# Performance work log

Hardware: AMD Instinct MI355X
Metric: run time of the kernel (lower is better)

The kernel has to match this reference:

```python
import jax, jax.numpy as jnp
import numpy as np

EPS = 1e-5

def inorm(x):
    # instance norm over time (last) axis; torch.std is unbiased (ddof=1)
    m = jnp.mean(x, axis=-1, keepdims=True)
    s = jnp.sqrt(jnp.var(x, axis=-1, ddof=1, keepdims=True))
    return (x - m) / (s + EPS)

def tinorm(x):
    # time-wise instance norm: normalize over channel axis (dim=1)
    m = jnp.mean(x, axis=1, keepdims=True)
    s = jnp.sqrt(jnp.var(x, axis=1, ddof=1, keepdims=True))
    return (x - m) / (s + EPS)

def adaptive_norm(src, trg, wq, wk, wv, norm_fn):
    # src, trg: [B,C,T]; wq/wk/wv: [out,in] as in nn.Linear
    temp = src.shape[1] ** 0.5
    q = jnp.einsum('bct,oc->bto', norm_fn(src), wq)        # [B,Ts,C]
    k = jnp.einsum('bct,oc->bto', norm_fn(trg), wk)        # [B,Tt,C]
    v = jnp.einsum('bct,oc->bto', trg, wv)                 # [B,Tt,C]
    attn = jax.nn.softmax(jnp.einsum('bsc,btc->bst', q / temp, k), axis=-1)
    mean = jnp.einsum('bst,btc->bsc', attn, v)             # attn-weighted mean
    var = jax.nn.relu(jnp.einsum('bst,btc->bsc', attn, v * v) - mean * mean)
    mean_c = jnp.mean(mean, axis=1)[:, :, None]            # [B,C,1]
    std_c = jnp.sqrt(jnp.mean(var, axis=1))[:, :, None]    # [B,C,1]
    return std_c * inorm(src) + mean_c

def sap(x, w, b):
    # self-attention pooling over axis 1; x: [B,N,C], w: [C], b: [1]
    a = jax.nn.softmax(jnp.einsum('bnc,c->bn', x, w) + b, axis=-1)
    return jnp.einsum('bnc,bn->bc', x, a)

def setup_inputs():
    key = jax.random.key(0)
    ks = jax.random.split(key, 24)
    B, C, Ts, Tt, S = 4, 512, 2048, 2048, 2048
    sc = 1.0 / np.sqrt(C).astype(np.float32)
    return {
        'src': jax.random.normal(ks[0], (B, C, Ts), jnp.float32),
        'trg': jax.random.normal(ks[1], (B, C, Tt), jnp.float32),
        'means': jax.random.normal(ks[2], (B, S, C), jnp.float32),
        'stds': jax.random.uniform(ks[3], (B, S, C), jnp.float32),
        'wq_t': jax.random.normal(ks[4], (C, C), jnp.float32) * sc,
        'wk_t': jax.random.normal(ks[5], (C, C), jnp.float32) * sc,
        'wv_t': jax.random.normal(ks[6], (C, C), jnp.float32) * sc,
        'wq_c': jax.random.normal(ks[7], (C, C), jnp.float32) * sc,
        'wk_c': jax.random.normal(ks[8], (C, C), jnp.float32) * sc,
        'wv_c': jax.random.normal(ks[9], (C, C), jnp.float32) * sc,
        'conv1_w': jax.random.normal(ks[10], (C, 2 * C), jnp.float32) * sc,
        'conv1_b': jax.random.normal(ks[11], (C,), jnp.float32) * 0.02,
        'conv2_w': jax.random.normal(ks[12], (C, C, 3), jnp.float32) * sc,
        'bn_g': jax.random.uniform(ks[13], (C,), jnp.float32, 0.5, 1.5),
        'bn_b': jax.random.normal(ks[14], (C,), jnp.float32) * 0.05,
        'bn_m': jax.random.normal(ks[15], (C,), jnp.float32) * 0.1,
        'bn_v': jax.random.uniform(ks[16], (C,), jnp.float32, 0.5, 1.5),
        'msap_w': jax.random.normal(ks[17], (C,), jnp.float32) * sc,
        'msap_b': jax.random.normal(ks[18], (1,), jnp.float32) * 0.02,
        'ssap_w': jax.random.normal(ks[19], (C,), jnp.float32) * sc,
        'ssap_b': jax.random.normal(ks[20], (1,), jnp.float32) * 0.02,
    }

def reference(src, trg, means, stds, wq_t, wk_t, wv_t, wq_c, wk_c, wv_c,
              conv1_w, conv1_b, conv2_w, bn_g, bn_b, bn_m, bn_v,
              msap_w, msap_b, ssap_w, ssap_b):
    src1 = adaptive_norm(src, trg, wq_t, wk_t, wv_t, tinorm)   # TAN
    src2 = adaptive_norm(src, trg, wq_c, wk_c, wv_c, inorm)    # CAN
    x = jnp.concatenate([src1, src2], axis=1)                  # [B,2C,T]
    # conv1: kernel_size=1 -> pointwise GEMM
    x = jnp.einsum('bct,oc->bot', x, conv1_w) + conv1_b[None, :, None]
    # conv2: Conv1d(k=3, pad=1, bias=False) + BatchNorm1d(eval) + ReLU
    x = jax.lax.conv_general_dilated(x, conv2_w, (1,), 'SAME',
                                     dimension_numbers=('NCH', 'OIH', 'NCH'))
    x = (x - bn_m[None, :, None]) * jax.lax.rsqrt(bn_v[None, :, None] + EPS)
    x = x * bn_g[None, :, None] + bn_b[None, :, None]
    x = jax.nn.relu(x)
    # GLAN
    mean = sap(means, msap_w, msap_b)[:, :, None]              # [B,C,1]
    std = sap(stds, ssap_w, ssap_b)[:, :, None]                # [B,C,1]
    return inorm(x) * std + mean
```

## Files before the change

kernel.cpp:

```cpp
#include <hip/hip_runtime.h>
#include <cstdint>
#include <cstddef>

#define B_ 4
#define C_ 512
#define T_ 2048
#define S_ 2048
#define EPSF 1e-5f

typedef __bf16 bf16;
typedef __attribute__((ext_vector_type(8))) __bf16 bf16x8;
typedef __attribute__((ext_vector_type(4))) float f32x4;

__device__ __forceinline__ bf16 f2b(float f){ return (bf16)f; }
__device__ __forceinline__ float b2f(bf16 h){ return (float)h; }

__device__ __forceinline__ void gl_lds16(const void* g, void* l){
  __builtin_amdgcn_global_load_lds((__attribute__((address_space(1))) void*)(g),
                                   (__attribute__((address_space(3))) void*)(l), 16, 0, 0);
}

__device__ __forceinline__ float wave_sum(float v){
#pragma unroll
  for (int o = 32; o; o >>= 1) v += __shfl_xor(v, o, 64);
  return v;
}
__device__ __forceinline__ float wave_max(float v){
#pragma unroll
  for (int o = 32; o; o >>= 1) v = fmaxf(v, __shfl_xor(v, o, 64));
  return v;
}

template<int EPI, int TNW>
__global__ void __launch_bounds__(256) gemm_nt(
    const bf16* __restrict__ A, const bf16* __restrict__ Bm, void* __restrict__ Cout,
    int K, int lda, int ldb, int ldc,
    long long sA, long long sB, long long sC, long long sCb,
    int zdivA, int zmodB, float scale,
    const float* __restrict__ rs, const float* __restrict__ rsh,
    const float* __restrict__ cbias,
    float* __restrict__ osum, float* __restrict__ osum2, long long sRs)
{
  constexpr int TN = TNW*32;
  __shared__ alignas(16) bf16 lA[128*64];
  __shared__ alignas(16) bf16 lB[TN*64];
  __shared__ float l_sh[128];
  const int tid = threadIdx.x;
  int z, m0, n0;
  if (EPI == 3) {
    const int id = blockIdx.x;
    z = id & 7;
    const int r = id >> 3;
    n0 = (r & 3) * TN;
    m0 = (r >> 2) * 128;
  } else {
    z = blockIdx.z; m0 = blockIdx.y*128; n0 = blockIdx.x*TN;
  }
  const bf16* Ab = A + (long long)(z / zdivA) * sA;
  const bf16* Bb = Bm + (long long)(z % zmodB) * sB;
  const int lane = tid & 63, wvi = tid >> 6;
  const int wm = wvi >> 1, wn = wvi & 1;

  f32x4 acc[4][TNW] = {};
  f32x4 accL[4] = {};
  bf16x8 vone;
#pragma unroll
  for (int j = 0; j < 8; ++j) vone[j] = f2b(1.f);

  const int lrow = tid >> 3;
  const int lcol = ((tid ^ lrow) & 7) * 8;
  const bf16* pa = Ab + (long long)(m0 + lrow)*lda + lcol;
  const bf16* pb = Bb + (long long)(n0 + lrow)*ldb + lcol;
  char* sa = (char*)lA + tid*16;
  char* sb = (char*)lB + tid*16;

  for (int k0 = 0; k0 < K; k0 += 64) {
#pragma unroll
    for (int it = 0; it < 4; ++it)
      gl_lds16(pa + (long long)it*32*lda + k0, sa + it*4096);
#pragma unroll
    for (int it = 0; it < TNW; ++it)
      gl_lds16(pb + (long long)it*32*ldb + k0, sb + it*4096);
    __syncthreads();
#pragma unroll
    for (int ks = 0; ks < 2; ++ks) {
      const int kq = ks*4 + (lane >> 4);
      bf16x8 af[4], bfr[TNW];
#pragma unroll
      for (int mt = 0; mt < 4; ++mt) {
        int r = wm*64 + mt*16 + (lane & 15);
        af[mt] = *(const bf16x8*)&lA[r*64 + ((kq ^ (r & 7))*8)];
      }
#pragma unroll
      for (int nt = 0; nt < TNW; ++nt) {
        int r = wn*(TNW*16) + nt*16 + (lane & 15);
        bfr[nt] = *(const bf16x8*)&lB[r*64 + ((kq ^ (r & 7))*8)];
      }
#pragma unroll
      for (int mt = 0; mt < 4; ++mt)
#pragma unroll
        for (int nt = 0; nt < TNW; ++nt)
          acc[mt][nt] = __builtin_amdgcn_mfma_f32_16x16x32_bf16(af[mt], bfr[nt], acc[mt][nt], 0, 0, 0);
      if (EPI == 3 && wn == 0) {
#pragma unroll
        for (int mt = 0; mt < 4; ++mt)
          accL[mt] = __builtin_amdgcn_mfma_f32_16x16x32_bf16(af[mt], vone, accL[mt], 0, 0, 0);
      }
    }
    __syncthreads();
  }

  if (EPI == 3) {
    if (wn == 0 && (lane & 15) == 0) {
#pragma unroll
      for (int mt = 0; mt < 4; ++mt)
#pragma unroll
        for (int i = 0; i < 4; ++i)
          l_sh[wm*64 + mt*16 + (lane >> 4)*4 + i] = accL[mt][i];
    }
    __syncthreads();
    if (n0 == 0 && tid < 128)
      ((float*)Cout)[(long long)z*sC + m0 + tid] = l_sh[tid];
    float linv[4][4];
#pragma unroll
    for (int mt = 0; mt < 4; ++mt)
#pragma unroll
      for (int i = 0; i < 4; ++i)
        linv[mt][i] = 1.f / l_sh[wm*64 + mt*16 + (lane >> 4)*4 + i];
    float* red1 = (float*)lA;
    float* red2 = red1 + 4*TNW*16;
    float s1[TNW], s2[TNW];
#pragma unroll
    for (int nt = 0; nt < TNW; ++nt) {
      s1[nt] = 0.f; s2[nt] = 0.f;
#pragma unroll
      for (int mt = 0; mt < 4; ++mt)
#pragma unroll
        for (int i = 0; i < 4; ++i) {
          float v = acc[mt][nt][i] * linv[mt][i];
          s1[nt] += v; s2[nt] += v*v;
        }
      s1[nt] += __shfl_xor(s1[nt], 16, 64);
      s1[nt] += __shfl_xor(s1[nt], 32, 64);
      s2[nt] += __shfl_xor(s2[nt], 16, 64);
      s2[nt] += __shfl_xor(s2[nt], 32, 64);
    }
    if (lane < 16) {
#pragma unroll
      for (int nt = 0; nt < TNW; ++nt) {
        red1[(wvi*TNW + nt)*16 + lane] = s1[nt];
        red2[(wvi*TNW + nt)*16 + lane] = s2[nt];
      }
    }
    __syncthreads();
    if (tid < 2*TN) {
      const int which = tid >= TN;
      const int col = tid - which*TN;
      const int wn2 = col / (TNW*16), rem = col % (TNW*16);
      const float* rr = which ? red2 : red1;
      float v = rr[wn2*(TNW*16) + rem] + rr[(2+wn2)*(TNW*16) + rem];
      float* dst = which ? osum2 : osum;
      atomicAdd(&dst[sCb*z + n0 + col], v);
    }
    return;
  }

  const int cr = (lane >> 4)*4, cc = lane & 15;
#pragma unroll
  for (int mt = 0; mt < 4; ++mt) {
#pragma unroll
    for (int i = 0; i < 4; ++i) {
      const int mm = m0 + wm*64 + mt*16 + cr + i;
      float rsum = 0.f, rsum2 = 0.f;
#pragma unroll
      for (int nt = 0; nt < TNW; ++nt) {
        const int nn = n0 + wn*(TNW*16) + nt*16 + cc;
        float v = acc[mt][nt][i];
        const long long co = sC*z + (long long)mm*ldc + nn;
        if (EPI == 0) {
          v *= scale;
          if (cbias) v += cbias[sCb*z + nn];
          ((bf16*)Cout)[co] = f2b(v);
        } else if (EPI == 2) {
          v = fmaxf(v*rs[mm] + rsh[mm], 0.f);
          ((float*)Cout)[co] = v;
          rsum += v; rsum2 += v*v;
        } else if (EPI == 5) {
          ((bf16*)Cout)[co] = f2b(__expf(v));
        }
      }
      if (EPI == 2) {
        rsum += __shfl_xor(rsum, 1, 64); rsum += __shfl_xor(rsum, 2, 64);
        rsum += __shfl_xor(rsum, 4, 64); rsum += __shfl_xor(rsum, 8, 64);
        rsum2 += __shfl_xor(rsum2, 1, 64); rsum2 += __shfl_xor(rsum2, 2, 64);
        rsum2 += __shfl_xor(rsum2, 4, 64); rsum2 += __shfl_xor(rsum2, 8, 64);
        if (cc == 0) {
          atomicAdd(&osum[(long long)z*sRs + mm], rsum);
          atomicAdd(&osum2[(long long)z*sRs + mm], rsum2);
        }
      }
    }
  }
}

__global__ void __launch_bounds__(256) row_stats_k(const float* __restrict__ X1,
    const float* __restrict__ X2, float* __restrict__ Mo, float* __restrict__ So, int n1)
{
  __shared__ float r1[4], r2[4];
  const int row = blockIdx.x;
  const float* x = (row < n1) ? X1 + (long long)row*T_ : X2 + (long long)(row-n1)*T_;
  float s1 = 0.f, s2 = 0.f;
  for (int i = threadIdx.x; i < T_; i += 256){ float v = x[i]; s1 += v; s2 += v*v; }
  s1 = wave_sum(s1); s2 = wave_sum(s2);
  const int lane = threadIdx.x & 63, w = threadIdx.x >> 6;
  if (!lane){ r1[w] = s1; r2[w] = s2; }
  __syncthreads();
  if (threadIdx.x == 0){
    s1 = r1[0]+r1[1]+r1[2]+r1[3];
    s2 = r2[0]+r2[1]+r2[2]+r2[3];
    float m = s1 * (1.f/T_);
    float var = (s2 - s1*m) * (1.f/(T_-1));
    Mo[row] = m; So[row] = sqrtf(fmaxf(var, 0.f));
  }
}

__global__ void __launch_bounds__(256) col_stats_k(const float* __restrict__ src,
    const float* __restrict__ trg, float* __restrict__ Mo, float* __restrict__ So)
{
  __shared__ float r1[4][64], r2[4][64];
  const int z = blockIdx.y, t0 = blockIdx.x*64;
  const float* X = (z < B_) ? src : trg;
  const int b = z & (B_-1);
  const int tl = threadIdx.x & 63, cg = threadIdx.x >> 6;
  float s1 = 0.f, s2 = 0.f;
  for (int c = cg; c < C_; c += 4) {
    float v = X[((long long)b*C_ + c)*T_ + t0 + tl];
    s1 += v; s2 += v*v;
  }
  r1[cg][tl] = s1; r2[cg][tl] = s2;
  __syncthreads();
  if (cg == 0) {
    s1 = r1[0][tl]+r1[1][tl]+r1[2][tl]+r1[3][tl];
    s2 = r2[0][tl]+r2[1][tl]+r2[2][tl]+r2[3][tl];
    float m = s1 * (1.f/C_);
    float var = (s2 - s1*m) * (1.f/(C_-1));
    Mo[z*T_ + t0 + tl] = m;
    So[z*T_ + t0 + tl] = sqrtf(fmaxf(var, 0.f));
  }
}

__global__ void __launch_bounds__(256) transform_k(const float* __restrict__ src,
    const float* __restrict__ trg,
    const float* __restrict__ tnm, const float* __restrict__ tns,
    const float* __restrict__ inm, const float* __restrict__ ins,
    bf16* __restrict__ NSt, bf16* __restrict__ NSc,
    bf16* __restrict__ NTt, bf16* __restrict__ NTc, bf16* __restrict__ TTr)
{
  __shared__ float tile[32][33];
  const int z = blockIdx.z, t0 = blockIdx.x*32, c0 = blockIdx.y*32;
  const int is_t = z >= B_, b = z & (B_-1);
  const float* X = is_t ? trg : src;
  const int tx = threadIdx.x, ty = threadIdx.y;
#pragma unroll
  for (int r = 0; r < 4; ++r) {
    int ci = ty + r*8;
    tile[ci][tx] = X[((long long)b*C_ + c0 + ci)*T_ + t0 + tx];
  }
  __syncthreads();
#pragma unroll
  for (int r = 0; r < 4; ++r) {
    int tj = ty + r*8, ci = tx;
    float v = tile[ci][tj];
    int gt = t0 + tj, gc = c0 + ci;
    float a = (v - tnm[z*T_ + gt]) / (tns[z*T_ + gt] + EPSF);
    float d = (v - inm[z*C_ + gc]) / (ins[z*C_ + gc] + EPSF);
    long long o = ((long long)b*T_ + gt)*C_ + gc;
    if (is_t) { NTt[o] = f2b(a); NTc[o] = f2b(d); TTr[o] = f2b(v); }
    else      { NSt[o] = f2b(a); NSc[o] = f2b(d); }
  }
}

__global__ void __launch_bounds__(256) softmax_row_k(const float* __restrict__ X, float* __restrict__ O)
{
  __shared__ float red[4];
  const long long row = blockIdx.x;
  const float* x = X + row*T_ + threadIdx.x*8;
  float v[8];
  f32x4 a0 = *(const f32x4*)x;
  f32x4 a1 = *(const f32x4*)(x + 4);
#pragma unroll
  for (int j = 0; j < 4; ++j){ v[j] = a0[j]; v[4+j] = a1[j]; }
  float m = -3.4e38f;
#pragma unroll
  for (int j = 0; j < 8; ++j) m = fmaxf(m, v[j]);
  m = wave_max(m);
  const int lane = threadIdx.x & 63, w = threadIdx.x >> 6;
  if (!lane) red[w] = m;
  __syncthreads();
  m = fmaxf(fmaxf(red[0], red[1]), fmaxf(red[2], red[3]));
  __syncthreads();
  float s = 0.f;
#pragma unroll
  for (int j = 0; j < 8; ++j){ v[j] = __expf(v[j] - m); s += v[j]; }
  s = wave_sum(s);
  if (!lane) red[w] = s;
  __syncthreads();
  s = red[0]+red[1]+red[2]+red[3];
  const float inv = 1.f/s;
  float* o = O + row*T_ + threadIdx.x*8;
#pragma unroll
  for (int j = 0; j < 8; ++j) o[j] = v[j]*inv;
}

__global__ void __launch_bounds__(256) colsum_k(const bf16* __restrict__ P,
    const float* __restrict__ l, float* __restrict__ cs)
{
  __shared__ float linv[256];
  const int t = blockIdx.x*256 + threadIdx.x;
  const int z = blockIdx.z;
  const long long s0 = (long long)blockIdx.y*256;
  linv[threadIdx.x] = 1.f / l[(long long)z*S_ + s0 + threadIdx.x];
  __syncthreads();
  const bf16* p = P + ((long long)z*S_ + s0)*T_ + t;
  float a = 0.f;
  for (int s = 0; s < 256; ++s) a += b2f(p[(long long)s*T_]) * linv[s];
  atomicAdd(&cs[z*T_ + t], a);
}

__global__ void __launch_bounds__(256) vv_fin_k(const float* __restrict__ cs,
    const bf16* __restrict__ VT, const float* __restrict__ msum,
    const float* __restrict__ m2sum, float* __restrict__ meanc, float* __restrict__ stdc)
{
  __shared__ float r1[4];
  const int c = blockIdx.x, z = blockIdx.y;
  const bf16* vr = VT + ((long long)z*C_ + c)*T_;
  const float* w = cs + z*T_;
  float a = 0.f;
  for (int t = threadIdx.x; t < T_; t += 256){ float v = b2f(vr[t]); a += w[t]*v*v; }
  a = wave_sum(a);
  const int lane = threadIdx.x & 63, wq = threadIdx.x >> 6;
  if (!lane) r1[wq] = a;
  __syncthreads();
  if (threadIdx.x == 0){
    a = r1[0]+r1[1]+r1[2]+r1[3];
    const int idx = z*C_ + c;
    meanc[idx] = msum[idx] * (1.f/S_);
    float var = (a - m2sum[idx]) * (1.f/S_);
    stdc[idx] = sqrtf(fmaxf(var, 0.f));
  }
}

__global__ void __launch_bounds__(256) weff_k(const float* __restrict__ w1,
    const float* __restrict__ b1, const float* __restrict__ sdt, const float* __restrict__ sdc,
    const float* __restrict__ mct, const float* __restrict__ mcc,
    bf16* __restrict__ Weff, float* __restrict__ beff)
{
  __shared__ float r1[4];
  const int o = blockIdx.x, b = blockIdx.y;
  float accb = 0.f;
  for (int c = threadIdx.x; c < C_; c += 256) {
    float wa = w1[o*2*C_ + c], wb = w1[o*2*C_ + C_ + c];
    Weff[((long long)(b*C_ + o))*C_ + c] = f2b(wa*sdt[b*C_+c] + wb*sdc[b*C_+c]);
    accb += wa*mct[b*C_+c] + wb*mcc[b*C_+c];
  }
  accb = wave_sum(accb);
  const int lane = threadIdx.x & 63, w = threadIdx.x >> 6;
  if (!lane) r1[w] = accb;
  __syncthreads();
  if (threadIdx.x == 0) beff[b*C_ + o] = b1[o] + r1[0]+r1[1]+r1[2]+r1[3];
}

__global__ void __launch_bounds__(256) prep_k(
    const float* __restrict__ a0, const float* __restrict__ a1,
    const float* __restrict__ a2, const float* __restrict__ a3,
    const float* __restrict__ a4, const float* __restrict__ a5,
    bf16* __restrict__ WQb,
    const float* __restrict__ w2, const float* __restrict__ g,
    const float* __restrict__ be, const float* __restrict__ mu,
    const float* __restrict__ va, bf16* __restrict__ W2r,
    float* __restrict__ bnsc, float* __restrict__ bnsh,
    bf16* __restrict__ x1p, float* __restrict__ zbase)
{
  const int bid = blockIdx.x, tid = threadIdx.x;
  if (bid < 6144) {
    const int i = bid*256 + tid;
    const int slot = i >> 18;
    const float* srcs[6] = {a0,a1,a2,a3,a4,a5};
    const float sc = (slot < 2) ? 0.044194173824159216f : 1.f;
    WQb[i] = f2b(srcs[slot][i & 262143] * sc);
  } else if (bid < 6656) {
    const int o = bid - 6144;
    for (int c = tid; c < C_; c += 256)
#pragma unroll
      for (int dt = 0; dt < 3; ++dt)
        W2r[(long long)o*3*C_ + dt*C_ + c] = f2b(w2[((long long)o*C_ + c)*3 + dt]);
    if (tid == 0) {
      float s = g[o] * rsqrtf(va[o] + EPSF);
      bnsc[o] = s;
      bnsh[o] = be[o] - mu[o]*s;
    }
  } else if (bid < 6672) {
    const int i = (bid - 6656)*256 + tid;
    const int b = i >> 10, rem = i & 1023;
    const long long row = (rem >> 9) ? (T_+1) : 0;
    const int c = rem & (C_-1);
    x1p[((long long)b*(T_+2) + row)*C_ + c] = f2b(0.f);
  } else {
    zbase[(bid - 6672)*256 + tid] = 0.f;
  }
}

__global__ void __launch_bounds__(256) sap_logit_k(const float* __restrict__ means,
    const float* __restrict__ stds, const float* __restrict__ mw, const float* __restrict__ sw,
    const float* __restrict__ mb, const float* __restrict__ sb, float* __restrict__ out)
{
  const int n = blockIdx.x*4 + (threadIdx.x >> 6);
  const int z = blockIdx.y;
  const int sel = z >= B_, b = z & (B_-1);
  const float* x = sel ? stds : means;
  const float* w = sel ? sw : mw;
  const int lane = threadIdx.x & 63;
  const float* p = x + ((long long)b*S_ + n)*C_;
  float a = 0.f;
  for (int c = lane; c < C_; c += 64) a += p[c]*w[c];
  a = wave_sum(a);
  if (!lane) out[z*S_ + n] = a + (sel ? sb[0] : mb[0]);
}

__global__ void __launch_bounds__(256) sap_wsum_k(const float* __restrict__ means,
    const float* __restrict__ stds, const float* __restrict__ a, float* __restrict__ out)
{
  const int c = blockIdx.x*256 + threadIdx.x;
  const int z = blockIdx.z;
  const int sel = z >= B_, b = z & (B_-1);
  const float* x = sel ? stds : means;
  const long long n0 = (long long)blockIdx.y*256;
  const float* p = x + ((long long)b*S_ + n0)*C_ + c;
  const float* aw = a + z*S_ + n0;
  float acc = 0.f;
  for (int n = 0; n < 256; ++n) acc += p[(long long)n*C_] * aw[n];
  atomicAdd(&out[z*C_ + c], acc);
}

__global__ void __launch_bounds__(256) final_k(const float* __restrict__ y,
    const float* __restrict__ ysum, const float* __restrict__ y2sum,
    const float* __restrict__ sapms, float* __restrict__ out)
{
  const long long i = (long long)(blockIdx.x*256 + threadIdx.x) * 4;
  const long long r = i >> 11;
  const float s1 = ysum[r], s2 = y2sum[r];
  const float m = s1 * (1.f/T_);
  const float var = (s2 - s1*m) * (1.f/(T_-1));
  const float inv = 1.f/(sqrtf(fmaxf(var, 0.f)) + EPSF);
  const float mn = sapms[r], sd = sapms[B_*C_ + r];
  const f32x4 v = *(const f32x4*)(y + i);
  f32x4 o;
#pragma unroll
  for (int j = 0; j < 4; ++j) o[j] = (v[j] - m)*inv*sd + mn;
  *(f32x4*)(out + i) = o;
}

extern "C" void kernel_launch(void* const* d_in, const int* in_sizes, int n_in,
                              void* d_out, int out_size, void* d_ws, size_t ws_size,
                              hipStream_t stream)
{
  (void)in_sizes; (void)n_in; (void)out_size; (void)ws_size;
  const float* src    = (const float*)d_in[0];
  const float* trg    = (const float*)d_in[1];
  const float* means  = (const float*)d_in[2];
  const float* stds   = (const float*)d_in[3];
  const float* conv1w = (const float*)d_in[10];
  const float* conv1b = (const float*)d_in[11];
  const float* conv2w = (const float*)d_in[12];
  const float* bn_g   = (const float*)d_in[13];
  const float* bn_b   = (const float*)d_in[14];
  const float* bn_m   = (const float*)d_in[15];
  const float* bn_v   = (const float*)d_in[16];
  const float* msap_w = (const float*)d_in[17];
  const float* msap_b = (const float*)d_in[18];
  const float* ssap_w = (const float*)d_in[19];
  const float* ssap_b = (const float*)d_in[20];

  const long long BTC = (long long)B_*T_*C_;

  char* p = (char*)d_ws;
  auto take = [&](size_t n)->char*{ char* r = p; p += (n + 255) & ~(size_t)255; return r; };

  bf16* NSc = (bf16*)take(BTC*2);
  bf16* P2  = (bf16*)take((size_t)2*B_*S_*T_*2);
  bf16* NSt = P2;
  bf16* NTc = P2 + BTC;
  bf16* NTt = P2 + 2*BTC;
  bf16* TTr = P2 + 3*BTC;
  bf16* QK4 = (bf16*)take((size_t)4*BTC*2);
  bf16* VT2 = (bf16*)take((size_t)2*BTC*2);
  bf16* WQb = (bf16*)take((size_t)6*C_*C_*2);
  bf16* Weff= (bf16*)take((size_t)B_*C_*C_*2);
  bf16* W2r = (bf16*)take((size_t)C_*3*C_*2);
  bf16* x1p = (bf16*)take((size_t)B_*(T_+2)*C_*2);
  float* y  = (float*)take((size_t)B_*C_*T_*4);
  float* colsum = (float*)take(2*B_*T_*4);
  float* msum   = (float*)take(2*B_*C_*4);
  float* m2sum  = (float*)take(2*B_*C_*4);
  float* sapms  = (float*)take(2*B_*C_*4);
  float* lrow   = (float*)take(2*B_*S_*4);
  float* ysum   = (float*)take(B_*C_*4);
  float* y2sum  = (float*)take(B_*C_*4);
  float* tnm = (float*)take(2*B_*T_*4);
  float* tns = (float*)take(2*B_*T_*4);
  float* inm = (float*)take(2*B_*C_*4);
  float* ins = (float*)take(2*B_*C_*4);
  float* meanc = (float*)take(2*B_*C_*4);
  float* stdc  = (float*)take(2*B_*C_*4);
  float* beff  = (float*)take(B_*C_*4);
  float* bnsc  = (float*)take(C_*4);
  float* bnsh  = (float*)take(C_*4);
  float* sapl  = (float*)take(2*B_*S_*4);
  float* sapa  = (float*)take(2*B_*S_*4);

  dim3 blk(256);

  prep_k<<<6864, blk, 0, stream>>>((const float*)d_in[7], (const float*)d_in[4],
      (const float*)d_in[8], (const float*)d_in[5], (const float*)d_in[9],
      (const float*)d_in[6], WQb, conv2w, bn_g, bn_b, bn_m, bn_v, W2r, bnsc, bnsh,
      x1p, colsum);
  row_stats_k<<<2*B_*C_, blk, 0, stream>>>(src, trg, inm, ins, B_*C_);
  col_stats_k<<<dim3(T_/64, 2*B_), blk, 0, stream>>>(src, trg, tnm, tns);
  transform_k<<<dim3(T_/32, C_/32, 2*B_), dim3(32,8), 0, stream>>>(src, trg,
      tnm, tns, inm, ins, NSt, NSc, NTt, NTc, TTr);

  gemm_nt<0,4><<<dim3(C_/128, (B_*T_)/128, 4), blk, 0, stream>>>(NSc, WQb, QK4,
      C_, C_, C_, C_, BTC, (long long)C_*C_, BTC, 0, 1, 8, 1.f,
      nullptr, nullptr, nullptr, nullptr, nullptr, 0);
  gemm_nt<0,2><<<dim3(T_/64, C_/128, 8), blk, 0, stream>>>(WQb + (size_t)4*C_*C_, TTr, VT2,
      C_, C_, C_, T_, (long long)C_*C_, (long long)T_*C_, (long long)C_*T_, 0, 4, 4, 1.f,
      nullptr, nullptr, nullptr, nullptr, nullptr, 0);
  gemm_nt<5,4><<<dim3(T_/128, T_/128, 8), blk, 0, stream>>>(QK4, QK4 + 2*BTC, P2,
      C_, C_, C_, T_, (long long)T_*C_, (long long)T_*C_, (long long)S_*T_, 0, 1, 8, 1.f,
      nullptr, nullptr, nullptr, nullptr, nullptr, 0);
  gemm_nt<3,4><<<dim3(512, 1, 1), blk, 0, stream>>>(P2, VT2, lrow,
      T_, T_, T_, 0, (long long)S_*T_, (long long)C_*T_, S_, C_, 1, 8, 1.f,
      nullptr, nullptr, nullptr, msum, m2sum, 0);
  colsum_k<<<dim3(T_/256, S_/256, 8), blk, 0, stream>>>(P2, lrow, colsum);
  vv_fin_k<<<dim3(C_, 2*B_), blk, 0, stream>>>(colsum, VT2, msum, m2sum, meanc, stdc);

  weff_k<<<dim3(C_, B_), blk, 0, stream>>>(conv1w, conv1b,
      stdc + B_*C_, stdc, meanc + B_*C_, meanc, Weff, beff);
  gemm_nt<0,2><<<dim3(C_/64, T_/128, B_), blk, 0, stream>>>(NSc, Weff, x1p + C_,
      C_, C_, C_, C_, (long long)T_*C_, (long long)C_*C_, (long long)(T_+2)*C_, C_,
      1, 8, 1.f, nullptr, nullptr, beff, nullptr, nullptr, 0);
  gemm_nt<2,2><<<dim3(T_/64, C_/128, B_), blk, 0, stream>>>(W2r, x1p, y,
      3*C_, 3*C_, C_, T_, 0, (long long)(T_+2)*C_, (long long)C_*T_, 0,
      1, 8, 1.f, bnsc, bnsh, nullptr, ysum, y2sum, C_);

  sap_logit_k<<<dim3(S_/4, 2*B_), blk, 0, stream>>>(means, stds, msap_w, ssap_w,
      msap_b, ssap_b, sapl);
  softmax_row_k<<<2*B_, blk, 0, stream>>>(sapl, sapa);
  sap_wsum_k<<<dim3(C_/256, S_/256, 2*B_), blk, 0, stream>>>(means, stds, sapa, sapms);

  final_k<<<4096, blk, 0, stream>>>(y, ysum, y2sum, sapms, (float*)d_out);
}
```

Measured before the change: 455.4 us.

## Swizzle GEMM block order, merge stats kernels, vectorize reductions, widen grids

Generalizes the z-interleaved block swizzle to the V projection and QK^T GEMMs so consecutive blocks share the same operand tiles across batches. Row and column statistics are merged into one launch, and row stats use float4 loads. colsum, vv_fin and sap_logit move to 8-wide vector loads, with colsum using shorter S chunks across more blocks. sap_wsum uses smaller chunks to get more parallelism. In exchange there are more atomics and changed L2 access patterns.

```diff
diff --git a/kernel.cpp b/kernel.cpp
--- a/kernel.cpp
+++ b/kernel.cpp
@@ -31,12 +31,12 @@
   return v;
 }
 
-template<int EPI, int TNW>
+template<int EPI, int TNW, int SWZ>
 __global__ void __launch_bounds__(256) gemm_nt(
     const bf16* __restrict__ A, const bf16* __restrict__ Bm, void* __restrict__ Cout,
     int K, int lda, int ldb, int ldc,
     long long sA, long long sB, long long sC, long long sCb,
-    int zdivA, int zmodB, float scale,
+    int zdivA, int zmodB, int nblk, float scale,
     const float* __restrict__ rs, const float* __restrict__ rsh,
     const float* __restrict__ cbias,
     float* __restrict__ osum, float* __restrict__ osum2, long long sRs)
@@ -44,15 +44,15 @@
   constexpr int TN = TNW*32;
   __shared__ alignas(16) bf16 lA[128*64];
   __shared__ alignas(16) bf16 lB[TN*64];
-  __shared__ float l_sh[128];
+  __shared__ float l_sh[EPI == 3 ? 128 : 4];
   const int tid = threadIdx.x;
   int z, m0, n0;
-  if (EPI == 3) {
+  if (SWZ) {
     const int id = blockIdx.x;
     z = id & 7;
     const int r = id >> 3;
-    n0 = (r & 3) * TN;
-    m0 = (r >> 2) * 128;
+    n0 = (r % nblk) * TN;
+    m0 = (r / nblk) * 128;
   } else {
     z = blockIdx.z; m0 = blockIdx.y*128; n0 = blockIdx.x*TN;
   }
@@ -203,49 +203,56 @@
   }
 }
 
-__global__ void __launch_bounds__(256) row_stats_k(const float* __restrict__ X1,
-    const float* __restrict__ X2, float* __restrict__ Mo, float* __restrict__ So, int n1)
-{
-  __shared__ float r1[4], r2[4];
-  const int row = blockIdx.x;
-  const float* x = (row < n1) ? X1 + (long long)row*T_ : X2 + (long long)(row-n1)*T_;
-  float s1 = 0.f, s2 = 0.f;
-  for (int i = threadIdx.x; i < T_; i += 256){ float v = x[i]; s1 += v; s2 += v*v; }
-  s1 = wave_sum(s1); s2 = wave_sum(s2);
-  const int lane = threadIdx.x & 63, w = threadIdx.x >> 6;
-  if (!lane){ r1[w] = s1; r2[w] = s2; }
-  __syncthreads();
-  if (threadIdx.x == 0){
-    s1 = r1[0]+r1[1]+r1[2]+r1[3];
-    s2 = r2[0]+r2[1]+r2[2]+r2[3];
-    float m = s1 * (1.f/T_);
-    float var = (s2 - s1*m) * (1.f/(T_-1));
-    Mo[row] = m; So[row] = sqrtf(fmaxf(var, 0.f));
-  }
-}
-
-__global__ void __launch_bounds__(256) col_stats_k(const float* __restrict__ src,
-    const float* __restrict__ trg, float* __restrict__ Mo, float* __restrict__ So)
-{
-  __shared__ float r1[4][64], r2[4][64];
-  const int z = blockIdx.y, t0 = blockIdx.x*64;
-  const float* X = (z < B_) ? src : trg;
-  const int b = z & (B_-1);
-  const int tl = threadIdx.x & 63, cg = threadIdx.x >> 6;
-  float s1 = 0.f, s2 = 0.f;
-  for (int c = cg; c < C_; c += 4) {
-    float v = X[((long long)b*C_ + c)*T_ + t0 + tl];
-    s1 += v; s2 += v*v;
-  }
-  r1[cg][tl] = s1; r2[cg][tl] = s2;
-  __syncthreads();
-  if (cg == 0) {
-    s1 = r1[0][tl]+r1[1][tl]+r1[2][tl]+r1[3][tl];
-    s2 = r2[0][tl]+r2[1][tl]+r2[2][tl]+r2[3][tl];
-    float m = s1 * (1.f/C_);
-    float var = (s2 - s1*m) * (1.f/(C_-1));
-    Mo[z*T_ + t0 + tl] = m;
-    So[z*T_ + t0 + tl] = sqrtf(fmaxf(var, 0.f));
+__global__ void __launch_bounds__(256) instats_k(const float* __restrict__ src,
+    const float* __restrict__ trg, float* __restrict__ inm, float* __restrict__ ins,
+    float* __restrict__ tnm, float* __restrict__ tns)
+{
+  const int bid = blockIdx.x, tid = threadIdx.x;
+  if (bid < 4096) {
+    __shared__ float r1[4], r2[4];
+    const int row = bid;
+    const float* x = (row < B_*C_) ? src + (long long)row*T_
+                                   : trg + (long long)(row - B_*C_)*T_;
+    float s1 = 0.f, s2 = 0.f;
+#pragma unroll
+    for (int h = 0; h < 2; ++h) {
+      f32x4 v = *(const f32x4*)(x + h*1024 + tid*4);
+#pragma unroll
+      for (int j = 0; j < 4; ++j){ s1 += v[j]; s2 += v[j]*v[j]; }
+    }
+    s1 = wave_sum(s1); s2 = wave_sum(s2);
+    const int lane = tid & 63, w = tid >> 6;
+    if (!lane){ r1[w] = s1; r2[w] = s2; }
+    __syncthreads();
+    if (tid == 0){
+      s1 = r1[0]+r1[1]+r1[2]+r1[3];
+      s2 = r2[0]+r2[1]+r2[2]+r2[3];
+      float m = s1 * (1.f/T_);
+      float var = (s2 - s1*m) * (1.f/(T_-1));
+      inm[row] = m; ins[row] = sqrtf(fmaxf(var, 0.f));
+    }
+  } else {
+    __shared__ float r1[4][64], r2[4][64];
+    const int cid = bid - 4096;
+    const int z = cid >> 5, t0 = (cid & 31)*64;
+    const float* X = (z < B_) ? src : trg;
+    const int b = z & (B_-1);
+    const int tl = tid & 63, cg = tid >> 6;
+    float s1 = 0.f, s2 = 0.f;
+    for (int c = cg; c < C_; c += 4) {
+      float v = X[((long long)b*C_ + c)*T_ + t0 + tl];
+      s1 += v; s2 += v*v;
+    }
+    r1[cg][tl] = s1; r2[cg][tl] = s2;
+    __syncthreads();
+    if (cg == 0) {
+      s1 = r1[0][tl]+r1[1][tl]+r1[2][tl]+r1[3][tl];
+      s2 = r2[0][tl]+r2[1][tl]+r2[2][tl]+r2[3][tl];
+      float m = s1 * (1.f/C_);
+      float var = (s2 - s1*m) * (1.f/(C_-1));
+      tnm[z*T_ + t0 + tl] = m;
+      tns[z*T_ + t0 + tl] = sqrtf(fmaxf(var, 0.f));
+    }
   }
 }
 
@@ -315,16 +322,25 @@
 __global__ void __launch_bounds__(256) colsum_k(const bf16* __restrict__ P,
     const float* __restrict__ l, float* __restrict__ cs)
 {
-  __shared__ float linv[256];
-  const int t = blockIdx.x*256 + threadIdx.x;
-  const int z = blockIdx.z;
-  const long long s0 = (long long)blockIdx.y*256;
-  linv[threadIdx.x] = 1.f / l[(long long)z*S_ + s0 + threadIdx.x];
-  __syncthreads();
-  const bf16* p = P + ((long long)z*S_ + s0)*T_ + t;
-  float a = 0.f;
-  for (int s = 0; s < 256; ++s) a += b2f(p[(long long)s*T_]) * linv[s];
-  atomicAdd(&cs[z*T_ + t], a);
+  __shared__ float linv[32];
+  const int id = blockIdx.x;
+  const int z = id & 7;
+  const long long s0 = (long long)(id >> 3) * 32;
+  const int tid = threadIdx.x;
+  if (tid < 32) linv[tid] = 1.f / l[(long long)z*S_ + s0 + tid];
+  __syncthreads();
+  const int t0 = tid*8;
+  const bf16* p = P + ((long long)z*S_ + s0)*T_ + t0;
+  float a[8] = {};
+#pragma unroll 4
+  for (int s = 0; s < 32; ++s) {
+    bf16x8 v = *(const bf16x8*)(p + (long long)s*T_);
+    const float w = linv[s];
+#pragma unroll
+    for (int j = 0; j < 8; ++j) a[j] += b2f(v[j]) * w;
+  }
+#pragma unroll
+  for (int j = 0; j < 8; ++j) atomicAdd(&cs[z*T_ + t0 + j], a[j]);
 }
 
 __global__ void __launch_bounds__(256) vv_fin_k(const float* __restrict__ cs,
@@ -333,15 +349,23 @@
 {
   __shared__ float r1[4];
   const int c = blockIdx.x, z = blockIdx.y;
-  const bf16* vr = VT + ((long long)z*C_ + c)*T_;
-  const float* w = cs + z*T_;
+  const int tid = threadIdx.x;
+  const bf16* vr = VT + ((long long)z*C_ + c)*T_ + tid*8;
+  const float* w = cs + z*T_ + tid*8;
+  bf16x8 v = *(const bf16x8*)vr;
+  f32x4 w0 = *(const f32x4*)w;
+  f32x4 w1 = *(const f32x4*)(w + 4);
   float a = 0.f;
-  for (int t = threadIdx.x; t < T_; t += 256){ float v = b2f(vr[t]); a += w[t]*v*v; }
+#pragma unroll
+  for (int j = 0; j < 4; ++j) {
+    float f0 = b2f(v[j]), f1 = b2f(v[4+j]);
+    a += w0[j]*f0*f0 + w1[j]*f1*f1;
+  }
   a = wave_sum(a);
-  const int lane = threadIdx.x & 63, wq = threadIdx.x >> 6;
+  const int lane = tid & 63, wq = tid >> 6;
   if (!lane) r1[wq] = a;
   __syncthreads();
-  if (threadIdx.x == 0){
+  if (tid == 0){
     a = r1[0]+r1[1]+r1[2]+r1[3];
     const int idx = z*C_ + c;
     meanc[idx] = msum[idx] * (1.f/S_);
@@ -414,15 +438,21 @@
     const float* __restrict__ stds, const float* __restrict__ mw, const float* __restrict__ sw,
     const float* __restrict__ mb, const float* __restrict__ sb, float* __restrict__ out)
 {
-  const int n = blockIdx.x*4 + (threadIdx.x >> 6);
+  const int tid = threadIdx.x;
+  const int n = blockIdx.x*4 + (tid >> 6);
   const int z = blockIdx.y;
   const int sel = z >= B_, b = z & (B_-1);
   const float* x = sel ? stds : means;
   const float* w = sel ? sw : mw;
-  const int lane = threadIdx.x & 63;
-  const float* p = x + ((long long)b*S_ + n)*C_;
+  const int lane = tid & 63;
+  const float* p = x + ((long long)b*S_ + n)*C_ + lane*8;
+  f32x4 p0 = *(const f32x4*)p;
+  f32x4 p1 = *(const f32x4*)(p + 4);
+  f32x4 w0 = *(const f32x4*)(w + lane*8);
+  f32x4 w1 = *(const f32x4*)(w + lane*8 + 4);
   float a = 0.f;
-  for (int c = lane; c < C_; c += 64) a += p[c]*w[c];
+#pragma unroll
+  for (int j = 0; j < 4; ++j) a += p0[j]*w0[j] + p1[j]*w1[j];
   a = wave_sum(a);
   if (!lane) out[z*S_ + n] = a + (sel ? sb[0] : mb[0]);
 }
@@ -434,11 +464,12 @@
   const int z = blockIdx.z;
   const int sel = z >= B_, b = z & (B_-1);
   const float* x = sel ? stds : means;
-  const long long n0 = (long long)blockIdx.y*256;
+  const long long n0 = (long long)blockIdx.y*64;
   const float* p = x + ((long long)b*S_ + n0)*C_ + c;
   const float* aw = a + z*S_ + n0;
   float acc = 0.f;
-  for (int n = 0; n < 256; ++n) acc += p[(long long)n*C_] * aw[n];
+#pragma unroll 4
+  for (int n = 0; n < 64; ++n) acc += p[(long long)n*C_] * aw[n];
   atomicAdd(&out[z*C_ + c], acc);
 }
 
@@ -524,39 +555,38 @@
       (const float*)d_in[8], (const float*)d_in[5], (const float*)d_in[9],
       (const float*)d_in[6], WQb, conv2w, bn_g, bn_b, bn_m, bn_v, W2r, bnsc, bnsh,
       x1p, colsum);
-  row_stats_k<<<2*B_*C_, blk, 0, stream>>>(src, trg, inm, ins, B_*C_);
-  col_stats_k<<<dim3(T_/64, 2*B_), blk, 0, stream>>>(src, trg, tnm, tns);
+  instats_k<<<4352, blk, 0, stream>>>(src, trg, inm, ins, tnm, tns);
   transform_k<<<dim3(T_/32, C_/32, 2*B_), dim3(32,8), 0, stream>>>(src, trg,
       tnm, tns, inm, ins, NSt, NSc, NTt, NTc, TTr);
 
-  gemm_nt<0,4><<<dim3(C_/128, (B_*T_)/128, 4), blk, 0, stream>>>(NSc, WQb, QK4,
-      C_, C_, C_, C_, BTC, (long long)C_*C_, BTC, 0, 1, 8, 1.f,
+  gemm_nt<0,4,0><<<dim3(C_/128, (B_*T_)/128, 4), blk, 0, stream>>>(NSc, WQb, QK4,
+      C_, C_, C_, C_, BTC, (long long)C_*C_, BTC, 0, 1, 8, 0, 1.f,
       nullptr, nullptr, nullptr, nullptr, nullptr, 0);
-  gemm_nt<0,2><<<dim3(T_/64, C_/128, 8), blk, 0, stream>>>(WQb + (size_t)4*C_*C_, TTr, VT2,
-      C_, C_, C_, T_, (long long)C_*C_, (long long)T_*C_, (long long)C_*T_, 0, 4, 4, 1.f,
+  gemm_nt<0,2,1><<<1024, blk, 0, stream>>>(WQb + (size_t)4*C_*C_, TTr, VT2,
+      C_, C_, C_, T_, (long long)C_*C_, (long long)T_*C_, (long long)C_*T_, 0, 4, 4, 32, 1.f,
       nullptr, nullptr, nullptr, nullptr, nullptr, 0);
-  gemm_nt<5,4><<<dim3(T_/128, T_/128, 8), blk, 0, stream>>>(QK4, QK4 + 2*BTC, P2,
-      C_, C_, C_, T_, (long long)T_*C_, (long long)T_*C_, (long long)S_*T_, 0, 1, 8, 1.f,
+  gemm_nt<5,4,1><<<2048, blk, 0, stream>>>(QK4, QK4 + 2*BTC, P2,
+      C_, C_, C_, T_, (long long)T_*C_, (long long)T_*C_, (long long)S_*T_, 0, 1, 8, 16, 1.f,
       nullptr, nullptr, nullptr, nullptr, nullptr, 0);
-  gemm_nt<3,4><<<dim3(512, 1, 1), blk, 0, stream>>>(P2, VT2, lrow,
-      T_, T_, T_, 0, (long long)S_*T_, (long long)C_*T_, S_, C_, 1, 8, 1.f,
+  gemm_nt<3,4,1><<<512, blk, 0, stream>>>(P2, VT2, lrow,
+      T_, T_, T_, 0, (long long)S_*T_, (long long)C_*T_, S_, C_, 1, 8, 4, 1.f,
       nullptr, nullptr, nullptr, msum, m2sum, 0);
-  colsum_k<<<dim3(T_/256, S_/256, 8), blk, 0, stream>>>(P2, lrow, colsum);
+  colsum_k<<<512, blk, 0, stream>>>(P2, lrow, colsum);
   vv_fin_k<<<dim3(C_, 2*B_), blk, 0, stream>>>(colsum, VT2, msum, m2sum, meanc, stdc);
 
   weff_k<<<dim3(C_, B_), blk, 0, stream>>>(conv1w, conv1b,
       stdc + B_*C_, stdc, meanc + B_*C_, meanc, Weff, beff);
-  gemm_nt<0,2><<<dim3(C_/64, T_/128, B_), blk, 0, stream>>>(NSc, Weff, x1p + C_,
+  gemm_nt<0,2,0><<<dim3(C_/64, T_/128, B_), blk, 0, stream>>>(NSc, Weff, x1p + C_,
       C_, C_, C_, C_, (long long)T_*C_, (long long)C_*C_, (long long)(T_+2)*C_, C_,
-      1, 8, 1.f, nullptr, nullptr, beff, nullptr, nullptr, 0);
-  gemm_nt<2,2><<<dim3(T_/64, C_/128, B_), blk, 0, stream>>>(W2r, x1p, y,
+      1, 8, 0, 1.f, nullptr, nullptr, beff, nullptr, nullptr, 0);
+  gemm_nt<2,2,0><<<dim3(T_/64, C_/128, B_), blk, 0, stream>>>(W2r, x1p, y,
       3*C_, 3*C_, C_, T_, 0, (long long)(T_+2)*C_, (long long)C_*T_, 0,
-      1, 8, 1.f, bnsc, bnsh, nullptr, ysum, y2sum, C_);
+      1, 8, 0, 1.f, bnsc, bnsh, nullptr, ysum, y2sum, C_);
 
   sap_logit_k<<<dim3(S_/4, 2*B_), blk, 0, stream>>>(means, stds, msap_w, ssap_w,
       msap_b, ssap_b, sapl);
   softmax_row_k<<<2*B_, blk, 0, stream>>>(sapl, sapa);
-  sap_wsum_k<<<dim3(C_/256, S_/256, 2*B_), blk, 0, stream>>>(means, stds, sapa, sapms);
+  sap_wsum_k<<<dim3(C_/256, S_/64, 2*B_), blk, 0, stream>>>(means, stds, sapa, sapms);
 
   final_k<<<4096, blk, 0, stream>>>(y, ysum, y2sum, sapms, (float*)d_out);
 }
```

Measured after the change: 465.8 us. 1.02x slower.
